# Optimization experiments

Measured on AMD Instinct MI355X. Metric: run time of the kernel, lower is better.

Reference implementation:

```python
import jax, jax.numpy as jnp
import numpy as np
from jax import lax

EPS = 1e-6
B, C, F, K = 64, 512, 1024, 3

def rmsnorm2d(x, w):
    # normalize over channel dim (axis=1), learnable per-channel scale
    inv = lax.rsqrt(jnp.mean(x * x, axis=1, keepdims=True) + EPS)
    return x * inv * w[None, :, None, None]

def pointwise(x, W, b):
    # 1x1 conv == per-pixel matmul: [B,C,H,F] x [O,C] -> [B,O,H,F]
    return jnp.einsum('bchf,oc->bohf', x, W) + b[None, :, None, None]

def depthwise_band(x, W, b):
    # depthwise conv, kernel (1,K), same padding along freq axis
    y = lax.conv_general_dilated(
        x, W,
        window_strides=(1, 1),
        padding=((0, 0), (K // 2, K // 2)),
        dimension_numbers=('NCHW', 'OIHW', 'NCHW'),
        feature_group_count=C)
    return y + b[None, :, None, None]

def setup_inputs() -> dict:
    key = jax.random.key(0)
    ks = jax.random.split(key, 6)
    s = 0.02
    return {
        'x_t': jax.random.normal(ks[0], (B, C, 1, F), jnp.float32),
        'h_prev': jax.random.normal(ks[1], (B, C, 1, F), jnp.float32),
        'in_norm_w': jnp.ones((C,), jnp.float32),
        'hid_norm_w': jnp.ones((C,), jnp.float32),
        'out_norm_w': jnp.ones((C,), jnp.float32),
        'xW': jax.random.normal(ks[2], (3 * C, C), jnp.float32) * s,
        'xb': jnp.zeros((3 * C,), jnp.float32),
        'hmixW': jax.random.normal(ks[3], (C, 1, 1, K), jnp.float32) * s,
        'hmixb': jnp.zeros((C,), jnp.float32),
        'hW': jax.random.normal(ks[4], (3 * C, C), jnp.float32) * s,
        'hb': jnp.zeros((3 * C,), jnp.float32),
    }

def reference(x_t, h_prev, in_norm_w, hid_norm_w, out_norm_w,
              xW, xb, hmixW, hmixb, hW, hb):
    xg = pointwise(rmsnorm2d(x_t, in_norm_w), xW, xb)            # [B,3C,1,F]
    hg = pointwise(depthwise_band(rmsnorm2d(h_prev, hid_norm_w), hmixW, hmixb), hW, hb)
    xr, xz, xn = jnp.split(xg, 3, axis=1)
    hr, hz, hn = jnp.split(hg, 3, axis=1)
    reset = jax.nn.sigmoid(xr + hr)
    update = jax.nn.sigmoid(xz + hz)
    cand = jnp.tanh(xn + reset * hn)
    h_new = (1.0 - update) * cand + update * h_prev
    return rmsnorm2d(h_new + x_t, out_norm_w)
```

## Files before the change

### kernel.cpp

```cpp
#include <hip/hip_runtime.h>

typedef __attribute__((ext_vector_type(8))) short short8;
typedef __attribute__((ext_vector_type(4))) float f32x4;
typedef __attribute__((ext_vector_type(4))) unsigned short u16x4;
typedef unsigned short u16;
typedef unsigned int u32;

#define EPSV 1e-6f

__device__ __forceinline__ u16 f2bf(float f){
  u32 u = __float_as_uint(f);
  u = u + 0x7fffu + ((u >> 16) & 1u);
  return (u16)(u >> 16);
}
__device__ __forceinline__ float bf2f(u16 h){
  return __uint_as_float(((u32)h) << 16);
}
__device__ __forceinline__ float sigm(float v){ return 1.f/(1.f + __expf(-v)); }
__device__ __forceinline__ float tanh_fast(float g){
  float e = __expf(-2.f*fabsf(g));
  return copysignf((1.f - e)/(1.f + e), g);
}
__device__ __forceinline__ void gload_lds16(const void* g, void* l){
  __builtin_amdgcn_global_load_lds(
      (const __attribute__((address_space(1))) u32*)g,
      (__attribute__((address_space(3))) u32*)l, 16, 0, 0);
}

#define WS_WXB   0u
#define WS_WHB   1572864u
#define WS_CB    3145728u
#define WS_SSQP  3153920u
#define WS_SBF   7348224u
#define WS_NEED  74457088u

extern "C" __global__ void wprep(const float* __restrict__ xW, const float* __restrict__ hW,
                                 const float* __restrict__ inw, const float* __restrict__ hidw,
                                 const float* __restrict__ xb, const float* __restrict__ hmixb,
                                 const float* __restrict__ hb,
                                 u16* __restrict__ xWb, u16* __restrict__ hWb,
                                 float* __restrict__ cb){
  __shared__ float red[4];
  const int n = blockIdx.x;
  const int tid = threadIdx.x;
  float pb = 0.f;
  for (int k = tid; k < 512; k += 256){
    float xw = xW[n*512 + k], hw = hW[n*512 + k];
    xWb[n*512 + k] = f2bf(xw * inw[k]);
    hWb[n*512 + k] = f2bf(hw * hidw[k]);
    pb += hw * hmixb[k];
  }
  #pragma unroll
  for (int off = 1; off < 64; off <<= 1) pb += __shfl_xor(pb, off);
  if ((tid & 63) == 0) red[tid >> 6] = pb;
  __syncthreads();
  if (tid == 0){
    float dot = red[0] + red[1] + red[2] + red[3];
    if (n < 1024){ cb[n] = xb[n] + hb[n] + dot; }
    else         { cb[n] = xb[n]; cb[n + 512] = hb[n] + dot; }
  }
}

extern "C" __global__ void __launch_bounds__(256)
wbuild(const float* __restrict__ x, const float* __restrict__ h,
       const float* __restrict__ hmixW,
       u16* __restrict__ Ax, u16* __restrict__ Ahm)
{
  __shared__ float tile[32][264];
  __shared__ float invx_s[256];
  __shared__ float invh_s[258];
  __shared__ float hmw_s[1536];

  const int b = blockIdx.y, fc = blockIdx.x;
  const int f0 = fc*256;
  const int t = threadIdx.x;
  const int r = t >> 3, q = t & 7;

  for (int i = t; i < 1536; i += 256) hmw_s[i] = hmixW[i];

  float ssq = 0.f;
  for (int cc = 0; cc < 16; ++cc){
    __syncthreads();
    const float* src = x + ((size_t)(b*512 + cc*32 + r))*1024 + f0;
    #pragma unroll
    for (int i = 0; i < 8; ++i)
      *(f32x4*)&tile[r][q*4 + i*32] = *(const f32x4*)(src + q*4 + i*32);
    __syncthreads();
    float p = 0.f;
    #pragma unroll
    for (int rr = 0; rr < 32; ++rr){ float v = tile[rr][t]; p += v*v; }
    ssq += p;
  }
  invx_s[t] = rsqrtf(ssq*(1.f/512.f) + EPSV);
  for (int cc = 0; cc < 16; ++cc){
    __syncthreads();
    const float* src = x + ((size_t)(b*512 + cc*32 + r))*1024 + f0;
    #pragma unroll
    for (int i = 0; i < 8; ++i)
      *(f32x4*)&tile[r][q*4 + i*32] = *(const f32x4*)(src + q*4 + i*32);
    __syncthreads();
    #pragma unroll
    for (int it = 0; it < 4; ++it){
      int id = it*256 + t;
      int pix = id >> 2, c8 = (id & 3)*8;
      float iv = invx_s[pix];
      short8 pk;
      #pragma unroll
      for (int j = 0; j < 8; ++j) pk[j] = (short)f2bf(tile[c8+j][pix]*iv);
      *(short8*)(Ax + ((size_t)(b*1024 + f0 + pix))*512 + cc*32 + c8) = pk;
    }
  }
  float ssqh = 0.f, ssqL = 0.f, ssqR = 0.f;
  for (int cc = 0; cc < 16; ++cc){
    __syncthreads();
    const float* src = h + ((size_t)(b*512 + cc*32 + r))*1024 + f0;
    #pragma unroll
    for (int i = 0; i < 8; ++i)
      *(f32x4*)&tile[r][q*4 + i*32] = *(const f32x4*)(src + q*4 + i*32);
    if (t < 32){
      tile[t][256] = (f0 > 0) ? h[((size_t)(b*512 + cc*32 + t))*1024 + f0 - 1] : 0.f;
    } else if (t < 64){
      int rr = t - 32;
      tile[rr][257] = (f0 + 256 < 1024) ? h[((size_t)(b*512 + cc*32 + rr))*1024 + f0 + 256] : 0.f;
    }
    __syncthreads();
    float p = 0.f;
    #pragma unroll
    for (int rr = 0; rr < 32; ++rr){ float v = tile[rr][t]; p += v*v; }
    ssqh += p;
    if (t == 0){ float p2=0.f; for (int rr=0; rr<32; ++rr){ float v=tile[rr][256]; p2+=v*v; } ssqL += p2; }
    if (t == 1){ float p2=0.f; for (int rr=0; rr<32; ++rr){ float v=tile[rr][257]; p2+=v*v; } ssqR += p2; }
  }
  invh_s[1 + t] = rsqrtf(ssqh*(1.f/512.f) + EPSV);
  if (t == 0) invh_s[0]   = rsqrtf(ssqL*(1.f/512.f) + EPSV);
  if (t == 1) invh_s[257] = rsqrtf(ssqR*(1.f/512.f) + EPSV);
  for (int cc = 0; cc < 16; ++cc){
    __syncthreads();
    const float* src = h + ((size_t)(b*512 + cc*32 + r))*1024 + f0;
    #pragma unroll
    for (int i = 0; i < 8; ++i)
      *(f32x4*)&tile[r][q*4 + i*32] = *(const f32x4*)(src + q*4 + i*32);
    if (t < 32){
      tile[t][256] = (f0 > 0) ? h[((size_t)(b*512 + cc*32 + t))*1024 + f0 - 1] : 0.f;
    } else if (t < 64){
      int rr = t - 32;
      tile[rr][257] = (f0 + 256 < 1024) ? h[((size_t)(b*512 + cc*32 + rr))*1024 + f0 + 256] : 0.f;
    }
    __syncthreads();
    #pragma unroll
    for (int it = 0; it < 4; ++it){
      int id = it*256 + t;
      int pix = id >> 2, c8 = (id & 3)*8;
      int colL = (pix == 0)   ? 256 : (pix - 1);
      int colR = (pix == 255) ? 257 : (pix + 1);
      float iL = invh_s[pix], iC = invh_s[pix+1], iR = invh_s[pix+2];
      short8 pk;
      #pragma unroll
      for (int j = 0; j < 8; ++j){
        int c = c8 + j;
        int cg = cc*32 + c;
        float v = hmw_s[cg*3+0]*tile[c][colL]*iL
                + hmw_s[cg*3+1]*tile[c][pix ]*iC
                + hmw_s[cg*3+2]*tile[c][colR]*iR;
        pk[j] = (short)f2bf(v);
      }
      *(short8*)(Ahm + ((size_t)(b*1024 + f0 + pix))*512 + cc*32 + c8) = pk;
    }
  }
}

extern "C" __global__ void __launch_bounds__(256, 2)
gemm_gates(const float* __restrict__ x, const float* __restrict__ h,
           const u16* __restrict__ Abase,
           const u16* __restrict__ xWb, const u16* __restrict__ hWb,
           const float* __restrict__ cb, const float* __restrict__ outw_unused,
           float* __restrict__ ssqp, u16* __restrict__ sbf)
{
  __shared__ __align__(16) char smem[45056];
  const int t = threadIdx.x;
  const int bid = blockIdx.x;
  const int swz = (bid & 7)*512 + (bid >> 3);
  const int mh = swz >> 4, ch = swz & 15;
  const int b = mh >> 2, f0 = (mh & 3)*256;
  const int c0 = ch*32;
  const int pixbase = b*1024 + f0;
  const int w = t >> 6, lane = t & 63, li = lane & 15, lg = lane >> 4;

  auto stage = [&](int tt, int buf){
    const int p = tt >> 4, kk = tt & 15;
    const u16* Asrc = Abase + (size_t)p*33554432;
    const u16* Wsrc = p ? hWb : xWb;
    char* adst = smem + buf*16384;
    #pragma unroll
    for (int uu = 0; uu < 4; ++uu){
      int u0 = (uu*4 + w)*64;
      int u = u0 + lane;
      int g = u >> 5, kq = (u >> 3) & 3, rr = g*8 + (u & 7);
      const u16* src = Asrc + ((size_t)(pixbase + rr))*512 + kk*32 + kq*8;
      gload_lds16(src, adst + u0*16);
    }
    char* bdst = smem + 32768 + buf*6144;
    {
      int u0 = w*64;
      int u = u0 + lane;
      int g = u >> 5, kq = (u >> 3) & 3, rb = g*8 + (u & 7);
      int n = (rb >> 5)*512 + c0 + (rb & 31);
      gload_lds16(Wsrc + (size_t)n*512 + kk*32 + kq*8, bdst + u0*16);
    }
    if (w < 2){
      int u0 = 256 + w*64;
      int u = u0 + lane;
      int g = u >> 5, kq = (u >> 3) & 3, rb = g*8 + (u & 7);
      int n = (rb >> 5)*512 + c0 + (rb & 31);
      gload_lds16(Wsrc + (size_t)n*512 + kk*32 + kq*8, bdst + u0*16);
    }
  };

  f32x4 accr[2][4] = {}, accz[2][4] = {}, accg1[2][4] = {}, accg2[2][4] = {};

  stage(0, 0);
  __syncthreads();
  int buf = 0;
  for (int tt = 0; tt < 32; ++tt){
    if (tt + 1 < 32) stage(tt + 1, buf ^ 1);
    const char* abase_l = smem + buf*16384;
    const char* bbase_l = smem + 32768 + buf*6144;
    short8 af[4];
    #pragma unroll
    for (int mf = 0; mf < 4; ++mf){
      int rA = w*64 + mf*16 + li;
      af[mf] = *(const short8*)(abase_l + ((rA >> 3) << 9) + (lg << 7) + ((rA & 7) << 4));
    }
    short8 bfr[2][3];
    #pragma unroll
    for (int ct = 0; ct < 2; ++ct)
      #pragma unroll
      for (int g = 0; g < 3; ++g){
        int rB = g*32 + ct*16 + li;
        bfr[ct][g] = *(const short8*)(bbase_l + ((rB >> 3) << 9) + (lg << 7) + ((rB & 7) << 4));
      }
    if (tt < 16){
      #pragma unroll
      for (int ct = 0; ct < 2; ++ct)
        #pragma unroll
        for (int mf = 0; mf < 4; ++mf){
          accr [ct][mf] = __builtin_amdgcn_mfma_f32_16x16x32_bf16(af[mf], bfr[ct][0], accr [ct][mf], 0,0,0);
          accz [ct][mf] = __builtin_amdgcn_mfma_f32_16x16x32_bf16(af[mf], bfr[ct][1], accz [ct][mf], 0,0,0);
          accg1[ct][mf] = __builtin_amdgcn_mfma_f32_16x16x32_bf16(af[mf], bfr[ct][2], accg1[ct][mf], 0,0,0);
        }
    } else {
      #pragma unroll
      for (int ct = 0; ct < 2; ++ct)
        #pragma unroll
        for (int mf = 0; mf < 4; ++mf){
          accr [ct][mf] = __builtin_amdgcn_mfma_f32_16x16x32_bf16(af[mf], bfr[ct][0], accr [ct][mf], 0,0,0);
          accz [ct][mf] = __builtin_amdgcn_mfma_f32_16x16x32_bf16(af[mf], bfr[ct][1], accz [ct][mf], 0,0,0);
          accg2[ct][mf] = __builtin_amdgcn_mfma_f32_16x16x32_bf16(af[mf], bfr[ct][2], accg2[ct][mf], 0,0,0);
        }
    }
    __syncthreads();
    buf ^= 1;
  }

  float (*stg)[264] = (float(*)[264])smem;
  float ps[4][4] = {};
  #pragma unroll
  for (int ct = 0; ct < 2; ++ct){
    const int c = c0 + ct*16 + li;
    const float cbr = cb[c], cbz = cb[512 + c], xbn = cb[1024 + c], hbn = cb[1536 + c];
    #pragma unroll
    for (int mf = 0; mf < 4; ++mf){
      const int f = f0 + w*64 + mf*16 + lg*4;
      const size_t gidx = ((size_t)(b*512 + c))*1024 + f;
      f32x4 hp = *(const f32x4*)(h + gidx);
      f32x4 xt = *(const f32x4*)(x + gidx);
      f32x4 sv;
      #pragma unroll
      for (int j = 0; j < 4; ++j){
        float rr = sigm(accr[ct][mf][j] + cbr);
        float zz = sigm(accz[ct][mf][j] + cbz);
        float g  = accg1[ct][mf][j] + xbn + rr*(accg2[ct][mf][j] + hbn);
        float th = tanh_fast(g);
        float s  = (1.f - zz)*th + zz*hp[j] + xt[j];
        sv[j] = s;
        ps[mf][j] += s*s;
      }
      *(f32x4*)&stg[ct*16 + li][w*64 + mf*16 + lg*4] = sv;
    }
  }
  #pragma unroll
  for (int off = 1; off < 16; off <<= 1)
    #pragma unroll
    for (int mf = 0; mf < 4; ++mf)
      #pragma unroll
      for (int j = 0; j < 4; ++j)
        ps[mf][j] += __shfl_xor(ps[mf][j], off);
  if (li == 0){
    #pragma unroll
    for (int mf = 0; mf < 4; ++mf){
      f32x4 v; v[0]=ps[mf][0]; v[1]=ps[mf][1]; v[2]=ps[mf][2]; v[3]=ps[mf][3];
      *(f32x4*)(ssqp + (size_t)ch*65536 + pixbase + w*64 + mf*16 + lg*4) = v;
    }
  }
  __syncthreads();
  {
    const int cl = t >> 3, seg = t & 7;
    u16* dst = sbf + ((size_t)(b*512 + c0 + cl))*1024 + f0 + seg*32;
    #pragma unroll
    for (int qq = 0; qq < 2; ++qq){
      f32x4 a0 = *(const f32x4*)&stg[cl][seg*32 + qq*16 + 0];
      f32x4 a1 = *(const f32x4*)&stg[cl][seg*32 + qq*16 + 4];
      f32x4 a2 = *(const f32x4*)&stg[cl][seg*32 + qq*16 + 8];
      f32x4 a3 = *(const f32x4*)&stg[cl][seg*32 + qq*16 + 12];
      short8 p0, p1;
      #pragma unroll
      for (int j = 0; j < 4; ++j){
        p0[j]   = (short)f2bf(a0[j]); p0[j+4] = (short)f2bf(a1[j]);
        p1[j]   = (short)f2bf(a2[j]); p1[j+4] = (short)f2bf(a3[j]);
      }
      *(short8*)(dst + qq*16)     = p0;
      *(short8*)(dst + qq*16 + 8) = p1;
    }
  }
}

extern "C" __global__ void __launch_bounds__(256)
outnorm(const float* __restrict__ ssqp, const u16* __restrict__ sbf,
        const float* __restrict__ outw, float* __restrict__ out)
{
  __shared__ float invf[1024];
  const int b = blockIdx.y, cch = blockIdx.x;
  const int t = threadIdx.x;
  f32x4 acc = {};
  #pragma unroll
  for (int p = 0; p < 16; ++p){
    f32x4 v = *(const f32x4*)(ssqp + (size_t)p*65536 + b*1024 + t*4);
    acc[0]+=v[0]; acc[1]+=v[1]; acc[2]+=v[2]; acc[3]+=v[3];
  }
  f32x4 iv;
  #pragma unroll
  for (int j = 0; j < 4; ++j) iv[j] = rsqrtf(acc[j]*(1.f/512.f) + EPSV);
  *(f32x4*)&invf[t*4] = iv;
  __syncthreads();
  for (int cl = 0; cl < 32; ++cl){
    const int c = cch*32 + cl;
    const float ow = outw[c];
    const u16* row = sbf + ((size_t)(b*512 + c))*1024;
    u16x4 sv = *(const u16x4*)(row + t*4);
    f32x4 o;
    #pragma unroll
    for (int j = 0; j < 4; ++j) o[j] = bf2f(sv[j]) * invf[t*4 + j] * ow;
    *(f32x4*)(out + ((size_t)(b*512 + c))*1024 + t*4) = o;
  }
}

#define FB_AXN_OFF 0
#define FB_AHM_OFF 32768
#define FB_RAW_OFF 65536
#define FB_PART_OFF 102400
#define FB_INVX_OFF 104512
#define FB_INVH_OFF 104640
#define FB_SSQ2_OFF 104784
#define FB_INVO_OFF 105936
#define FB_SMEM_BYTES 106112

extern "C" __global__ void fb_wconv(const float* __restrict__ xW, const float* __restrict__ hW,
                                    u16* __restrict__ xWb, u16* __restrict__ hWb){
  int i = blockIdx.x*256 + threadIdx.x;
  xWb[i] = f2bf(xW[i]);
  hWb[i] = f2bf(hW[i]);
}

extern "C" __global__ void __launch_bounds__(512, 2)
fb_gru(const float* __restrict__ x, const float* __restrict__ h,
       const float* __restrict__ inw, const float* __restrict__ hidw,
       const float* __restrict__ outw,
       const float* __restrict__ xb, const float* __restrict__ hmixWc,
       const float* __restrict__ hmixb, const float* __restrict__ hb,
       const u16* __restrict__ xWb, const u16* __restrict__ hWb,
       float* __restrict__ out)
{
  extern __shared__ __align__(16) char smem[];
  const int b  = blockIdx.y;
  const int f0 = blockIdx.x * 32;
  const int t  = threadIdx.x;
  u16* raw = (u16*)(smem + FB_RAW_OFF);
  float* part = (float*)(smem + FB_PART_OFF);
  {
    const int fq = t & 7, cb2 = t >> 3;
    #pragma unroll
    for (int pass = 0; pass < 8; ++pass){
      int c = pass*64 + cb2;
      f32x4 v = *(const f32x4*)(x + ((size_t)(b*512 + c))*1024 + f0 + fq*4);
      u16* d = raw + c*36 + fq*4;
      d[0] = f2bf(v[0]); d[1] = f2bf(v[1]); d[2] = f2bf(v[2]); d[3] = f2bf(v[3]);
    }
  }
  __syncthreads();
  {
    const int f = t & 31, cs = t >> 5;
    float p = 0.f;
    for (int i = 0; i < 32; ++i){ float v = bf2f(raw[(cs*32 + i)*36 + f]); p += v*v; }
    part[cs*33 + f] = p;
  }
  __syncthreads();
  if (t < 32){
    float s = 0.f;
    for (int i = 0; i < 16; ++i) s += part[i*33 + t];
    ((float*)(smem + FB_INVX_OFF))[t] = rsqrtf(s*(1.f/512.f) + EPSV);
  }
  __syncthreads();
  {
    const int f = t >> 4, cc = t & 15;
    const float iv = ((float*)(smem + FB_INVX_OFF))[f];
    #pragma unroll
    for (int it = 0; it < 4; ++it){
      int cbase = (cc + it*16)*8;
      short8 pk;
      #pragma unroll
      for (int j = 0; j < 8; ++j){
        float v = bf2f(raw[(cbase+j)*36 + f]) * iv * inw[cbase+j];
        pk[j] = (short)f2bf(v);
      }
      *(short8*)(smem + FB_AXN_OFF + f*1024 + ((cbase*2) ^ ((f&7)<<4))) = pk;
    }
  }
  __syncthreads();
  {
    const int fq = t & 7, cb2 = t >> 3;
    #pragma unroll
    for (int pass = 0; pass < 8; ++pass){
      int c = pass*64 + cb2;
      f32x4 v = *(const f32x4*)(h + ((size_t)(b*512 + c))*1024 + f0 + fq*4);
      u16* d = raw + c*36 + 1 + fq*4;
      d[0] = f2bf(v[0]); d[1] = f2bf(v[1]); d[2] = f2bf(v[2]); d[3] = f2bf(v[3]);
    }
    {
      int c = t;
      size_t base = ((size_t)(b*512 + c))*1024;
      float lv = (f0 > 0)          ? h[base + f0 - 1]  : 0.f;
      float rv = (f0 + 32 < 1024)  ? h[base + f0 + 32] : 0.f;
      raw[c*36 + 0]  = f2bf(lv);
      raw[c*36 + 33] = f2bf(rv);
    }
  }
  __syncthreads();
  {
    const int fw = t & 63, cs = t >> 6;
    if (fw < 34){
      float p = 0.f;
      for (int i = 0; i < 64; ++i){ float v = bf2f(raw[(cs*64 + i)*36 + fw]); p += v*v; }
      part[cs*35 + fw] = p;
    }
  }
  __syncthreads();
  if (t < 34){
    float s = 0.f;
    for (int i = 0; i < 8; ++i) s += part[i*35 + t];
    ((float*)(smem + FB_INVH_OFF))[t] = rsqrtf(s*(1.f/512.f) + EPSV);
  }
  __syncthreads();
  {
    const int fr = t >> 5, cc = t & 31;
    const float* invh = (const float*)(smem + FB_INVH_OFF);
    const float iL = invh[fr], iC = invh[fr + 1], iR = invh[fr + 2];
    #pragma unroll
    for (int it = 0; it < 2; ++it){
      const int cbase = (cc + it*32)*8;
      short8 o;
      #pragma unroll
      for (int j = 0; j < 8; ++j){
        int c = cbase + j;
        float hL = bf2f(raw[c*36 + fr])     * iL;
        float hC = bf2f(raw[c*36 + fr + 1]) * iC;
        float hR = bf2f(raw[c*36 + fr + 2]) * iR;
        float v = (hmixWc[c*3]*hL + hmixWc[c*3+1]*hC + hmixWc[c*3+2]*hR) * hidw[c] + hmixb[c];
        o[j] = (short)f2bf(v);
      }
      *(short8*)(smem + FB_AHM_OFF + fr*1024 + ((cbase*2) ^ ((fr&7)<<4))) = o;
    }
  }
  __syncthreads();
  const int wv = t >> 6, lane = t & 63, li = lane & 15, lg = lane >> 4;
  const int n0 = wv*64;
  f32x4 ar[2][4] = {}, az[2][4] = {}, axg[2][4] = {}, ahg[2][4] = {};
  #pragma unroll
  for (int src = 0; src < 2; ++src){
    const char* A = smem + (src ? FB_AHM_OFF : FB_AXN_OFF);
    const u16* W = src ? hWb : xWb;
    for (int k0 = 0; k0 < 512; k0 += 32){
      const int kb = (k0*2 + lg*16) ^ ((li & 7) << 4);
      short8 a0 = *(const short8*)(A + li*1024 + kb);
      short8 a1 = *(const short8*)(A + (li+16)*1024 + kb);
      #pragma unroll
      for (int nt = 0; nt < 4; ++nt){
        const u16* bp = W + (size_t)(n0 + nt*16 + li)*512 + k0 + lg*8;
        short8 br = *(const short8*)(bp);
        short8 bz = *(const short8*)(bp + 512*512);
        short8 bg = *(const short8*)(bp + 1024*512);
        ar[0][nt] = __builtin_amdgcn_mfma_f32_16x16x32_bf16(a0, br, ar[0][nt], 0,0,0);
        ar[1][nt] = __builtin_amdgcn_mfma_f32_16x16x32_bf16(a1, br, ar[1][nt], 0,0,0);
        az[0][nt] = __builtin_amdgcn_mfma_f32_16x16x32_bf16(a0, bz, az[0][nt], 0,0,0);
        az[1][nt] = __builtin_amdgcn_mfma_f32_16x16x32_bf16(a1, bz, az[1][nt], 0,0,0);
        if (src == 0){
          axg[0][nt] = __builtin_amdgcn_mfma_f32_16x16x32_bf16(a0, bg, axg[0][nt], 0,0,0);
          axg[1][nt] = __builtin_amdgcn_mfma_f32_16x16x32_bf16(a1, bg, axg[1][nt], 0,0,0);
        } else {
          ahg[0][nt] = __builtin_amdgcn_mfma_f32_16x16x32_bf16(a0, bg, ahg[0][nt], 0,0,0);
          ahg[1][nt] = __builtin_amdgcn_mfma_f32_16x16x32_bf16(a1, bg, ahg[1][nt], 0,0,0);
        }
      }
    }
  }
  float ps[8] = {0,0,0,0,0,0,0,0};
  #pragma unroll
  for (int nt = 0; nt < 4; ++nt){
    const int c = n0 + nt*16 + li;
    const float xbr = xb[c], xbz = xb[512+c], xbg = xb[1024+c];
    const float hbr = hb[c], hbz = hb[512+c], hbg = hb[1024+c];
    #pragma unroll
    for (int mt = 0; mt < 2; ++mt){
      const size_t idx = ((size_t)(b*512 + c))*1024 + f0 + mt*16 + lg*4;
      const f32x4 hp = *(const f32x4*)(h + idx);
      const f32x4 xt = *(const f32x4*)(x + idx);
      f32x4 sv;
      #pragma unroll
      for (int j = 0; j < 4; ++j){
        float rr = sigm(ar[mt][nt][j] + xbr + hbr);
        float zz = sigm(az[mt][nt][j] + xbz + hbz);
        float g  = axg[mt][nt][j] + xbg + rr*(ahg[mt][nt][j] + hbg);
        float th = tanh_fast(g);
        float hv = (1.f - zz)*th + zz*hp[j];
        float s  = hv + xt[j];
        sv[j] = s;
        ps[mt*4 + j] += s*s;
      }
      ar[mt][nt] = sv;
    }
  }
  #pragma unroll
  for (int off = 1; off < 16; off <<= 1){
    #pragma unroll
    for (int p = 0; p < 8; ++p) ps[p] += __shfl_xor(ps[p], off);
  }
  __syncthreads();
  float* stg = (float*)(smem + FB_AXN_OFF);
  #pragma unroll
  for (int nt = 0; nt < 4; ++nt){
    const int n = n0 + nt*16 + li;
    #pragma unroll
    for (int mt = 0; mt < 2; ++mt){
      const int m0 = mt*16 + lg*4;
      *(f32x4*)(stg + n*32 + (m0 ^ ((n & 7) << 2))) = ar[mt][nt];
    }
  }
  float* sq2 = (float*)(smem + FB_SSQ2_OFF);
  if (li == 0){
    #pragma unroll
    for (int p = 0; p < 8; ++p){
      int m = (p >> 2)*16 + lg*4 + (p & 3);
      sq2[m*9 + wv] = ps[p];
    }
  }
  __syncthreads();
  if (t < 32){
    float s = 0.f;
    for (int i = 0; i < 8; ++i) s += sq2[t*9 + i];
    ((float*)(smem + FB_INVO_OFF))[t] = rsqrtf(s*(1.f/512.f) + EPSV);
  }
  __syncthreads();
  {
    const float* invO = (const float*)(smem + FB_INVO_OFF);
    const int cb2 = t >> 3, chh = t & 7;
    #pragma unroll
    for (int pass = 0; pass < 8; ++pass){
      int c = pass*64 + cb2;
      int base = (chh*4) ^ ((c & 7) << 2);
      f32x4 v = *(const f32x4*)(stg + c*32 + base);
      float ow = outw[c];
      f32x4 o;
      #pragma unroll
      for (int j = 0; j < 4; ++j) o[j] = v[j] * invO[chh*4 + j] * ow;
      *(f32x4*)(out + ((size_t)(b*512 + c))*1024 + f0 + chh*4) = o;
    }
  }
}

extern "C" void kernel_launch(void* const* d_in, const int* in_sizes, int n_in,
                              void* d_out, int out_size, void* d_ws, size_t ws_size,
                              hipStream_t stream){
  (void)in_sizes; (void)n_in; (void)out_size;
  const float* x      = (const float*)d_in[0];
  const float* h      = (const float*)d_in[1];
  const float* inw    = (const float*)d_in[2];
  const float* hidw   = (const float*)d_in[3];
  const float* outw   = (const float*)d_in[4];
  const float* xW     = (const float*)d_in[5];
  const float* xb     = (const float*)d_in[6];
  const float* hmixW  = (const float*)d_in[7];
  const float* hmixb  = (const float*)d_in[8];
  const float* hW     = (const float*)d_in[9];
  const float* hb     = (const float*)d_in[10];

  if (ws_size >= (size_t)WS_NEED){
    u16*   xWb  = (u16*)((char*)d_ws + WS_WXB);
    u16*   hWb  = (u16*)((char*)d_ws + WS_WHB);
    float* cbw  = (float*)((char*)d_ws + WS_CB);
    float* ssqp = (float*)((char*)d_ws + WS_SSQP);
    u16*   sbf  = (u16*)((char*)d_ws + WS_SBF);
    u16*   Ax   = (u16*)d_out;
    u16*   Ahm  = Ax + 33554432;

    wprep<<<1536, 256, 0, stream>>>(xW, hW, inw, hidw, xb, hmixb, hb, xWb, hWb, cbw);
    wbuild<<<dim3(4, 64), 256, 0, stream>>>(x, h, hmixW, Ax, Ahm);
    gemm_gates<<<4096, 256, 0, stream>>>(x, h, Ax, xWb, hWb, cbw, outw, ssqp, sbf);
    outnorm<<<dim3(16, 64), 256, 0, stream>>>(ssqp, sbf, outw, (float*)d_out);
  } else {
    u16* xWb = (u16*)d_ws;
    u16* hWb = xWb + 786432;
    hipFuncSetAttribute(reinterpret_cast<const void*>(fb_gru),
                        hipFuncAttributeMaxDynamicSharedMemorySize, FB_SMEM_BYTES);
    fb_wconv<<<3072, 256, 0, stream>>>(xW, hW, xWb, hWb);
    dim3 grid(32, 64);
    fb_gru<<<grid, 512, FB_SMEM_BYTES, stream>>>(x, h, inw, hidw, outw,
                                                 xb, hmixW, hmixb, hb,
                                                 xWb, hWb, (float*)d_out);
  }
}
```

Measured before the change: 619.1 us.

## Load weight fragments directly from global and triple-buffer the activation tiles

```diff
diff --git a/kernel.cpp b/kernel.cpp
--- a/kernel.cpp
+++ b/kernel.cpp
@@ -173,10 +173,10 @@
 gemm_gates(const float* __restrict__ x, const float* __restrict__ h,
            const u16* __restrict__ Abase,
            const u16* __restrict__ xWb, const u16* __restrict__ hWb,
-           const float* __restrict__ cb, const float* __restrict__ outw_unused,
+           const float* __restrict__ cb,
            float* __restrict__ ssqp, u16* __restrict__ sbf)
 {
-  __shared__ __align__(16) char smem[45056];
+  __shared__ __align__(16) char smem[49152];
   const int t = threadIdx.x;
   const int bid = blockIdx.x;
   const int swz = (bid & 7)*512 + (bid >> 3);
@@ -189,7 +189,6 @@
   auto stage = [&](int tt, int buf){
     const int p = tt >> 4, kk = tt & 15;
     const u16* Asrc = Abase + (size_t)p*33554432;
-    const u16* Wsrc = p ? hWb : xWb;
     char* adst = smem + buf*16384;
     #pragma unroll
     for (int uu = 0; uu < 4; ++uu){
@@ -199,32 +198,14 @@
       const u16* src = Asrc + ((size_t)(pixbase + rr))*512 + kk*32 + kq*8;
       gload_lds16(src, adst + u0*16);
     }
-    char* bdst = smem + 32768 + buf*6144;
-    {
-      int u0 = w*64;
-      int u = u0 + lane;
-      int g = u >> 5, kq = (u >> 3) & 3, rb = g*8 + (u & 7);
-      int n = (rb >> 5)*512 + c0 + (rb & 31);
-      gload_lds16(Wsrc + (size_t)n*512 + kk*32 + kq*8, bdst + u0*16);
-    }
-    if (w < 2){
-      int u0 = 256 + w*64;
-      int u = u0 + lane;
-      int g = u >> 5, kq = (u >> 3) & 3, rb = g*8 + (u & 7);
-      int n = (rb >> 5)*512 + c0 + (rb & 31);
-      gload_lds16(Wsrc + (size_t)n*512 + kk*32 + kq*8, bdst + u0*16);
-    }
   };
 
   f32x4 accr[2][4] = {}, accz[2][4] = {}, accg1[2][4] = {}, accg2[2][4] = {};
 
-  stage(0, 0);
-  __syncthreads();
-  int buf = 0;
-  for (int tt = 0; tt < 32; ++tt){
-    if (tt + 1 < 32) stage(tt + 1, buf ^ 1);
+  auto body = [&](int tt, int buf){
+    const int p = tt >> 4, kk = tt & 15;
+    const u16* Wsrc = p ? hWb : xWb;
     const char* abase_l = smem + buf*16384;
-    const char* bbase_l = smem + 32768 + buf*6144;
     short8 af[4];
     #pragma unroll
     for (int mf = 0; mf < 4; ++mf){
@@ -235,11 +216,9 @@
     #pragma unroll
     for (int ct = 0; ct < 2; ++ct)
       #pragma unroll
-      for (int g = 0; g < 3; ++g){
-        int rB = g*32 + ct*16 + li;
-        bfr[ct][g] = *(const short8*)(bbase_l + ((rB >> 3) << 9) + (lg << 7) + ((rB & 7) << 4));
-      }
-    if (tt < 16){
+      for (int g = 0; g < 3; ++g)
+        bfr[ct][g] = *(const short8*)(Wsrc + ((size_t)(g*512 + c0 + ct*16 + li))*512 + kk*32 + lg*8);
+    if (p == 0){
       #pragma unroll
       for (int ct = 0; ct < 2; ++ct)
         #pragma unroll
@@ -258,8 +237,26 @@
           accg2[ct][mf] = __builtin_amdgcn_mfma_f32_16x16x32_bf16(af[mf], bfr[ct][2], accg2[ct][mf], 0,0,0);
         }
     }
-    __syncthreads();
-    buf ^= 1;
+  };
+
+  stage(0, 0);
+  stage(1, 1);
+  asm volatile("s_waitcnt vmcnt(4)" ::: "memory");
+  __builtin_amdgcn_sched_barrier(0);
+  __builtin_amdgcn_s_barrier();
+
+  for (int tt = 0; tt < 30; ++tt){
+    stage(tt + 2, (tt + 2) % 3);
+    body(tt, tt % 3);
+    asm volatile("s_waitcnt vmcnt(4)" ::: "memory");
+    __builtin_amdgcn_sched_barrier(0);
+    __builtin_amdgcn_s_barrier();
+  }
+  for (int tt = 30; tt < 32; ++tt){
+    body(tt, tt % 3);
+    asm volatile("s_waitcnt vmcnt(0)" ::: "memory");
+    __builtin_amdgcn_sched_barrier(0);
+    __builtin_amdgcn_s_barrier();
   }
 
   float (*stg)[264] = (float(*)[264])smem;
@@ -613,7 +610,7 @@
 
     wprep<<<1536, 256, 0, stream>>>(xW, hW, inw, hidw, xb, hmixb, hb, xWb, hWb, cbw);
     wbuild<<<dim3(4, 64), 256, 0, stream>>>(x, h, hmixW, Ax, Ahm);
-    gemm_gates<<<4096, 256, 0, stream>>>(x, h, Ax, xWb, hWb, cbw, outw, ssqp, sbf);
+    gemm_gates<<<4096, 256, 0, stream>>>(x, h, Ax, xWb, hWb, cbw, ssqp, sbf);
     outnorm<<<dim3(16, 64), 256, 0, stream>>>(ssqp, sbf, outw, (float*)d_out);
   } else {
     u16* xWb = (u16*)d_ws;
```

New measurement: 1.385 ms. 124% more time.
